# Kernel tuning notes

Measured on AMD Instinct MI355X. Metric: run time of the kernel, lower is better.

Reference implementation:

```python
import jax, jax.numpy as jnp
import numpy as np

N_HEADS = 16
EMBED_DIM = 1024
HEAD_DIM = EMBED_DIM // N_HEADS  # 64
SRC_LEN = 64  # shifted-causal mask: key j visible iff j <= i + SRC_LEN
THETA = 10000.0


def _rope_tables(T, D, dtype):
    # angles[t, p] = t / theta^(2p/D), p in [0, D/2)
    freqs = 1.0 / (THETA ** (jnp.arange(0, D, 2, dtype=jnp.float32) / D))  # [D/2]
    ang = jnp.arange(T, dtype=jnp.float32)[:, None] * freqs[None, :]       # [T, D/2]
    return jnp.cos(ang).astype(dtype), jnp.sin(ang).astype(dtype)


def _apply_rope(x, cos, sin):
    # x: [B, T, H, D]; pairs along last dim act as complex numbers
    B, T, H, D = x.shape
    xp = x.reshape(B, T, H, D // 2, 2)
    x0, x1 = xp[..., 0], xp[..., 1]
    c = cos[None, :, None, :]  # [1, T, 1, D/2]
    s = sin[None, :, None, :]
    o0 = x0 * c - x1 * s
    o1 = x0 * s + x1 * c
    return jnp.stack([o0, o1], axis=-1).reshape(B, T, H, D)


def setup_inputs() -> dict:
    key = jax.random.key(0)
    ks = jax.random.split(key, 9)
    B, T, C = 2, 2048, EMBED_DIM
    sc = 1.0 / np.sqrt(C)
    inp = {
        "x_1": jax.random.normal(ks[0], (B, T, C), dtype=jnp.float32),
        "x_2": jax.random.normal(ks[1], (B, T, C), dtype=jnp.float32),
        "wq": jax.random.normal(ks[2], (C, C), dtype=jnp.float32) * sc,
        "bq": jax.random.normal(ks[3], (C,), dtype=jnp.float32) * sc,
        "wk": jax.random.normal(ks[4], (C, C), dtype=jnp.float32) * sc,
        "bk": jax.random.normal(ks[5], (C,), dtype=jnp.float32) * sc,
        "wv": jax.random.normal(ks[6], (C, C), dtype=jnp.float32) * sc,
        "bv": jax.random.normal(ks[7], (C,), dtype=jnp.float32) * sc,
        "wp": jax.random.normal(ks[8], (C, C), dtype=jnp.float32) * sc,
    }
    return inp


def reference(x_1, x_2, wq, bq, wk, bk, wv, bv, wp):
    B, T, C = x_1.shape
    H, D = N_HEADS, HEAD_DIM
    q = (x_1 @ wq.T + bq).reshape(B, T, H, D)
    k = (x_2 @ wk.T + bk).reshape(B, T, H, D)
    v = (x_2 @ wv.T + bv).reshape(B, T, H, D)
    cos, sin = _rope_tables(T, D, x_1.dtype)
    q = _apply_rope(q, cos, sin)
    k = _apply_rope(k, cos, sin)
    # attention with shifted causal mask
    attn = jnp.einsum("bihd,bjhd->bhij", q, k) * (D ** -0.5)
    i = jnp.arange(T)
    mask = i[None, :] <= i[:, None] + SRC_LEN  # [T, T], True = visible
    attn = jnp.where(mask[None, None, :, :], attn, -jnp.inf)
    attn = jax.nn.softmax(attn, axis=-1)
    out = jnp.einsum("bhij,bjhd->bihd", attn, v).reshape(B, T, C)
    return out @ wp.T
```

## Files before the change

kernel.cpp:

```cpp
#include <hip/hip_runtime.h>
#include <hip/hip_bf16.h>

typedef __bf16 v8bf __attribute__((ext_vector_type(8)));
typedef float  v4f  __attribute__((ext_vector_type(4)));

#define T_LEN 2048
#define NH 16
#define HD 64
#define BH 32
#define C_DIM 1024
#define SCQ 0.1803368801111737f

#define WS_X1B  ((size_t)0)
#define WS_X2B  ((size_t)8  << 20)
#define WS_W    ((size_t)16 << 20)
#define WS_CTAB ((size_t)24 << 20)
#define WS_STAB (WS_CTAB + 262144)
#define WS_Q    ((size_t)25 << 20)
#define WS_K    ((size_t)33 << 20)
#define WS_VT   ((size_t)41 << 20)
#define WS_O    ((size_t)0)

__device__ __forceinline__ unsigned short f2bf(float f) {
  unsigned int u = __float_as_uint(f);
  u += 0x7fffu + ((u >> 16) & 1u);
  return (unsigned short)(u >> 16);
}
__device__ __forceinline__ float bf2f(unsigned short h) {
  return __uint_as_float(((unsigned int)h) << 16);
}

__device__ __forceinline__ float xg_max(float m) {
  m = fmaxf(m, __shfl_xor(m, 16, 64));
  m = fmaxf(m, __shfl_xor(m, 32, 64));
  return m;
}
__device__ __forceinline__ float xg_sum(float m) {
  m = m + __shfl_xor(m, 16, 64);
  m = m + __shfl_xor(m, 32, 64);
  return m;
}
__device__ __forceinline__ unsigned int packbf2(float lo, float hi) {
  return (unsigned int)f2bf(lo) | ((unsigned int)f2bf(hi) << 16);
}

__global__ __launch_bounds__(256) void cvt_kernel(
    const float* __restrict__ x1, const float* __restrict__ x2,
    const float* __restrict__ wq, const float* __restrict__ wk,
    const float* __restrict__ wv, const float* __restrict__ wp,
    unsigned short* __restrict__ x1b, unsigned short* __restrict__ x2b,
    unsigned short* __restrict__ wqb) {
  int i = blockIdx.x * 256 + threadIdx.x;
  if (i >= 3145728) return;
  const float* s; unsigned short* d; int off;
  if (i < 1048576) { s = x1; d = x1b; off = i; }
  else if (i < 2097152) { s = x2; d = x2b; off = i - 1048576; }
  else {
    int j = i - 2097152;
    int w = j >> 18;
    off = j & 262143;
    s = (w == 0) ? wq : (w == 1) ? wk : (w == 2) ? wv : wp;
    d = wqb + ((size_t)w * 1048576);
  }
  float4 v = ((const float4*)s)[off];
  ushort4 o;
  o.x = f2bf(v.x); o.y = f2bf(v.y); o.z = f2bf(v.z); o.w = f2bf(v.w);
  ((ushort4*)d)[off] = o;
}

__global__ __launch_bounds__(256) void tab_kernel(float* __restrict__ ctab,
                                                  float* __restrict__ stab) {
  int i = blockIdx.x * 256 + threadIdx.x;
  int t = i >> 5, f = i & 31;
  float freq = powf(10000.0f, -(float)f * (1.0f / 32.0f));
  float a = (float)t * freq;
  ctab[i] = cosf(a);
  stab[i] = sinf(a);
}

__global__ __launch_bounds__(256) void qk_gemm(
    const unsigned short* __restrict__ x1b, const unsigned short* __restrict__ x2b,
    const unsigned short* __restrict__ wall,
    const float* __restrict__ bq, const float* __restrict__ bk,
    const float* __restrict__ ctab, const float* __restrict__ stab,
    unsigned short* __restrict__ Qd, unsigned short* __restrict__ Kd) {
  int z = blockIdx.z;
  const unsigned short* A = (z == 0) ? x1b : x2b;
  const unsigned short* W = wall + (size_t)z * 1048576;
  const float* bias = (z == 0) ? bq : bk;
  unsigned short* dst = (z == 0) ? Qd : Kd;
  float scale = (z == 0) ? SCQ : 1.0f;

  __shared__ unsigned short lds[2][8192];
  int tid = threadIdx.x;
  int wave = tid >> 6, lane = tid & 63;
  int wm = wave >> 1, wn = wave & 1;
  int r = lane & 15, g = lane >> 4;
  int phys = blockIdx.y * (int)gridDim.x + blockIdx.x;
  int logical = (phys & 7) * 32 + (phys >> 3);
  int m0 = (logical >> 3) * 128, n0 = (logical & 7) * 128;
  int s3 = r & 3;

  v4f zero = {0.f, 0.f, 0.f, 0.f};
  v4f acc[4][4];
#pragma unroll
  for (int i = 0; i < 4; ++i)
#pragma unroll
    for (int j = 0; j < 4; ++j) acc[i][j] = zero;

  auto stage = [&](int b, int k0) {
    const unsigned short* Ab = A + (size_t)m0 * 1024 + k0;
    const unsigned short* Bb = W + (size_t)n0 * 1024 + k0;
#pragma unroll
    for (int it = 0; it < 2; ++it) {
      int c = it * 256 + tid;
      int row = c >> 2;
      int sc = (c & 3) ^ (row & 3);
      __builtin_amdgcn_global_load_lds(
          (const __attribute__((address_space(1))) void*)(Ab + (size_t)row * 1024 + sc * 8),
          (__attribute__((address_space(3))) void*)(&lds[b][0] + it * 2048 + wave * 512),
          16, 0, 0);
      __builtin_amdgcn_global_load_lds(
          (const __attribute__((address_space(1))) void*)(Bb + (size_t)row * 1024 + sc * 8),
          (__attribute__((address_space(3))) void*)(&lds[b][4096] + it * 2048 + wave * 512),
          16, 0, 0);
    }
  };

  stage(0, 0);
  asm volatile("s_waitcnt vmcnt(0)");
  __syncthreads();
  int cur = 0;

  for (int k0 = 0; k0 < 1024; k0 += 32) {
    if (k0 + 32 < 1024) stage(cur ^ 1, k0 + 32);
    v8bf af[4], bfr[4];
#pragma unroll
    for (int mf = 0; mf < 4; ++mf)
      af[mf] = *(const v8bf*)(&lds[cur][0] + (wm * 64 + mf * 16 + r) * 32 + ((g ^ s3) << 3));
#pragma unroll
    for (int nf = 0; nf < 4; ++nf)
      bfr[nf] = *(const v8bf*)(&lds[cur][4096] + (wn * 64 + nf * 16 + r) * 32 + ((g ^ s3) << 3));
#pragma unroll
    for (int mf = 0; mf < 4; ++mf)
#pragma unroll
      for (int nf = 0; nf < 4; ++nf)
        acc[mf][nf] = __builtin_amdgcn_mfma_f32_16x16x32_bf16(bfr[nf], af[mf], acc[mf][nf], 0, 0, 0);
    asm volatile("s_waitcnt vmcnt(0)");
    __syncthreads();
    cur ^= 1;
  }

#pragma unroll
  for (int mf = 0; mf < 4; ++mf) {
    int t = m0 + wm * 64 + mf * 16 + r;
    int b = t >> 11, tt = t & 2047;
#pragma unroll
    for (int nf = 0; nf < 4; ++nf) {
      int c0 = n0 + wn * 64 + nf * 16 + g * 4;
      int h = c0 >> 6, dh = c0 & 63;
      float4 b4 = *(const float4*)(bias + c0);
      int f0 = (dh >> 1);
      float2 cp = *(const float2*)(ctab + tt * 32 + f0);
      float2 sp = *(const float2*)(stab + tt * 32 + f0);
      float x0 = acc[mf][nf][0] + b4.x, x1 = acc[mf][nf][1] + b4.y;
      float x2 = acc[mf][nf][2] + b4.z, x3 = acc[mf][nf][3] + b4.w;
      ushort4 pk;
      pk.x = f2bf((x0 * cp.x - x1 * sp.x) * scale);
      pk.y = f2bf((x0 * sp.x + x1 * cp.x) * scale);
      pk.z = f2bf((x2 * cp.y - x3 * sp.y) * scale);
      pk.w = f2bf((x2 * sp.y + x3 * cp.y) * scale);
      *(ushort4*)(dst + (((size_t)(b * NH + h)) * T_LEN + tt) * HD + dh) = pk;
    }
  }
}

__global__ __launch_bounds__(256) void v_gemm(
    const unsigned short* __restrict__ x2b, const unsigned short* __restrict__ wv,
    const float* __restrict__ bv, unsigned short* __restrict__ VTd) {
  __shared__ unsigned short lds[2][8192];
  int tid = threadIdx.x;
  int wave = tid >> 6, lane = tid & 63;
  int wm = wave >> 1, wn = wave & 1;
  int r = lane & 15, g = lane >> 4;
  int phys = blockIdx.y * (int)gridDim.x + blockIdx.x;
  int logical = (phys & 7) * 32 + (phys >> 3);
  int m0 = (logical >> 3) * 128, n0 = (logical & 7) * 128;
  int s3 = r & 3;

  v4f zero = {0.f, 0.f, 0.f, 0.f};
  v4f acc[4][4];
#pragma unroll
  for (int i = 0; i < 4; ++i)
#pragma unroll
    for (int j = 0; j < 4; ++j) acc[i][j] = zero;

  auto stage = [&](int b, int k0) {
    const unsigned short* Ab = x2b + (size_t)m0 * 1024 + k0;
    const unsigned short* Bb = wv + (size_t)n0 * 1024 + k0;
#pragma unroll
    for (int it = 0; it < 2; ++it) {
      int c = it * 256 + tid;
      int row = c >> 2;
      int sc = (c & 3) ^ (row & 3);
      __builtin_amdgcn_global_load_lds(
          (const __attribute__((address_space(1))) void*)(Ab + (size_t)row * 1024 + sc * 8),
          (__attribute__((address_space(3))) void*)(&lds[b][0] + it * 2048 + wave * 512),
          16, 0, 0);
      __builtin_amdgcn_global_load_lds(
          (const __attribute__((address_space(1))) void*)(Bb + (size_t)row * 1024 + sc * 8),
          (__attribute__((address_space(3))) void*)(&lds[b][4096] + it * 2048 + wave * 512),
          16, 0, 0);
    }
  };

  stage(0, 0);
  asm volatile("s_waitcnt vmcnt(0)");
  __syncthreads();
  int cur = 0;

  for (int k0 = 0; k0 < 1024; k0 += 32) {
    if (k0 + 32 < 1024) stage(cur ^ 1, k0 + 32);
    v8bf af[4], bfr[4];
#pragma unroll
    for (int mf = 0; mf < 4; ++mf)
      af[mf] = *(const v8bf*)(&lds[cur][0] + (wm * 64 + mf * 16 + r) * 32 + ((g ^ s3) << 3));
#pragma unroll
    for (int nf = 0; nf < 4; ++nf)
      bfr[nf] = *(const v8bf*)(&lds[cur][4096] + (wn * 64 + nf * 16 + r) * 32 + ((g ^ s3) << 3));
#pragma unroll
    for (int mf = 0; mf < 4; ++mf)
#pragma unroll
      for (int nf = 0; nf < 4; ++nf)
        acc[mf][nf] = __builtin_amdgcn_mfma_f32_16x16x32_bf16(af[mf], bfr[nf], acc[mf][nf], 0, 0, 0);
    asm volatile("s_waitcnt vmcnt(0)");
    __syncthreads();
    cur ^= 1;
  }
#pragma unroll
  for (int nf = 0; nf < 4; ++nf) {
    int col = n0 + wn * 64 + nf * 16 + r;
    float bv_ = bv[col];
    int h = col >> 6, d = col & 63;
#pragma unroll
    for (int mf = 0; mf < 4; ++mf) {
      int row0 = m0 + wm * 64 + mf * 16 + g * 4;
      int b = row0 >> 11, t0 = row0 & 2047;
      ushort4 pk;
      pk.x = f2bf(acc[mf][nf][0] + bv_);
      pk.y = f2bf(acc[mf][nf][1] + bv_);
      pk.z = f2bf(acc[mf][nf][2] + bv_);
      pk.w = f2bf(acc[mf][nf][3] + bv_);
      *(ushort4*)(VTd + (((size_t)(b * NH + h)) * HD + d) * T_LEN + t0) = pk;
    }
  }
}

__global__ __launch_bounds__(256, 2) void attn_kernel(
    const unsigned short* __restrict__ Qd, const unsigned short* __restrict__ Kd,
    const unsigned short* __restrict__ VTd, unsigned short* __restrict__ Od) {
  int bh = blockIdx.x;
  int qt = (int)gridDim.y - 1 - (int)blockIdx.y;
  int tid = threadIdx.x, wave = tid >> 6, lane = tid & 63;
  int r = lane & 15, g = lane >> 4;
  int qb = qt * 128 + wave * 32;
  const unsigned short* Qp = Qd + (size_t)bh * T_LEN * HD;
  const unsigned short* Kp = Kd + (size_t)bh * T_LEN * HD;
  const unsigned short* Vp = VTd + (size_t)bh * HD * T_LEN;

  __shared__ unsigned short kv[2][2][4096];
  __shared__ unsigned short plds[4][1024];

  v8bf qf[2][2];
#pragma unroll
  for (int qs = 0; qs < 2; ++qs)
#pragma unroll
    for (int c = 0; c < 2; ++c)
      qf[qs][c] = *(const v8bf*)(Qp + (size_t)(qb + qs * 16 + r) * HD + c * 32 + g * 8);

  v4f zero = {0.f, 0.f, 0.f, 0.f};
  v4f oacc[2][4];
#pragma unroll
  for (int qs = 0; qs < 2; ++qs)
#pragma unroll
    for (int dt = 0; dt < 4; ++dt) oacc[qs][dt] = zero;
  float mi[2] = {-1e30f, -1e30f};
  float li[2] = {0.f, 0.f};

  int ktiles = 2 * qt + 3; if (ktiles > 32) ktiles = 32;

  auto stage = [&](int b, int kt) {
    int j0 = kt * 64;
    const unsigned short* Kt = Kp + (size_t)j0 * HD;
#pragma unroll
    for (int is = 0; is < 2; ++is) {
      int q = is * 256 + tid;
      int row = q >> 3, c = q & 7;
      int swc = (c ^ (row & 7)) << 3;
      __builtin_amdgcn_global_load_lds(
          (const __attribute__((address_space(1))) void*)(Kt + row * 64 + swc),
          (__attribute__((address_space(3))) void*)(&kv[b][0][0] + is * 2048 + wave * 512),
          16, 0, 0);
      __builtin_amdgcn_global_load_lds(
          (const __attribute__((address_space(1))) void*)(Vp + (size_t)row * T_LEN + j0 + swc),
          (__attribute__((address_space(3))) void*)(&kv[b][1][0] + is * 2048 + wave * 512),
          16, 0, 0);
    }
  };

  stage(0, 0);
  asm volatile("s_waitcnt vmcnt(0)");
  __syncthreads();
  int cur = 0;

  unsigned short* plw = &plds[wave][0];
  int s7 = r & 7;
  int s8 = s7 << 3;

  for (int kt = 0; kt < ktiles; ++kt) {
    if (kt + 1 < ktiles) stage(cur ^ 1, kt + 1);
    int j0 = kt * 64;
    const unsigned short* kb = &kv[cur][0][0];
    const unsigned short* vb = &kv[cur][1][0];
    v8bf kf0[4], kf1[4], vf0[4], vf1[4];
#pragma unroll
    for (int nt = 0; nt < 4; ++nt) {
      int row = (nt * 16 + r) * 64;
      kf0[nt] = *(const v8bf*)(kb + row + ((g ^ s7) << 3));
      kf1[nt] = *(const v8bf*)(kb + row + (((4 + g) ^ s7) << 3));
      vf0[nt] = *(const v8bf*)(vb + row + ((g ^ s7) << 3));
      vf1[nt] = *(const v8bf*)(vb + row + (((4 + g) ^ s7) << 3));
    }
#pragma unroll
    for (int qs = 0; qs < 2; ++qs) {
      int qmin = qb + qs * 16;
      if (j0 > qmin + 79) continue;
      v4f s[4];
#pragma unroll
      for (int nt = 0; nt < 4; ++nt) {
        v4f a = zero;
        a = __builtin_amdgcn_mfma_f32_16x16x32_bf16(kf0[nt], qf[qs][0], a, 0, 0, 0);
        a = __builtin_amdgcn_mfma_f32_16x16x32_bf16(kf1[nt], qf[qs][1], a, 0, 0, 0);
        s[nt] = a;
      }
      if (j0 + 63 > qmin + 64) {
        int qi64 = qmin + r + 64;
#pragma unroll
        for (int nt = 0; nt < 4; ++nt)
#pragma unroll
          for (int rg = 0; rg < 4; ++rg) {
            int kj = j0 + nt * 16 + g * 4 + rg;
            if (kj > qi64) s[nt][rg] = -1e30f;
          }
      }
      float m = s[0][0];
#pragma unroll
      for (int nt = 0; nt < 4; ++nt)
#pragma unroll
        for (int rg = 0; rg < 4; ++rg) m = fmaxf(m, s[nt][rg]);
      m = xg_max(m);
      float mn = fmaxf(mi[qs], m);
      float al = exp2f(mi[qs] - mn);
      mi[qs] = mn;
      float rs = 0.f;
#pragma unroll
      for (int nt = 0; nt < 4; ++nt)
#pragma unroll
        for (int rg = 0; rg < 4; ++rg) {
          float p = exp2f(s[nt][rg] - mn);
          s[nt][rg] = p;
          rs += p;
        }
      li[qs] = li[qs] * al + rs;
#pragma unroll
      for (int dt = 0; dt < 4; ++dt) oacc[qs][dt] *= al;
#pragma unroll
      for (int nt = 0; nt < 4; ++nt) {
        uint2 w2;
        w2.x = packbf2(s[nt][0], s[nt][1]);
        w2.y = packbf2(s[nt][2], s[nt][3]);
        *(uint2*)(plw + r * 64 + (((nt << 4) + (g << 2)) ^ s8)) = w2;
      }
      v8bf pb0 = *(const v8bf*)(plw + r * 64 + ((g ^ s7) << 3));
      v8bf pb1 = *(const v8bf*)(plw + r * 64 + (((4 + g) ^ s7) << 3));
#pragma unroll
      for (int dt = 0; dt < 4; ++dt) {
        oacc[qs][dt] = __builtin_amdgcn_mfma_f32_16x16x32_bf16(vf0[dt], pb0, oacc[qs][dt], 0, 0, 0);
        oacc[qs][dt] = __builtin_amdgcn_mfma_f32_16x16x32_bf16(vf1[dt], pb1, oacc[qs][dt], 0, 0, 0);
      }
    }
    asm volatile("s_waitcnt vmcnt(0)");
    __syncthreads();
    cur ^= 1;
  }
#pragma unroll
  for (int qs = 0; qs < 2; ++qs) {
    float rli = 1.0f / xg_sum(li[qs]);
#pragma unroll
    for (int dt = 0; dt < 4; ++dt) {
      ushort4 pk;
      pk.x = f2bf(oacc[qs][dt][0] * rli);
      pk.y = f2bf(oacc[qs][dt][1] * rli);
      pk.z = f2bf(oacc[qs][dt][2] * rli);
      pk.w = f2bf(oacc[qs][dt][3] * rli);
      *(ushort4*)(Od + ((size_t)bh * T_LEN + qb + qs * 16 + r) * HD + dt * 16 + g * 4) = pk;
    }
  }
}

__global__ __launch_bounds__(256) void proj_gemm(
    const unsigned short* __restrict__ Ob, const unsigned short* __restrict__ Wpb,
    float* __restrict__ out) {
  __shared__ unsigned short lds[2][8192];
  int tid = threadIdx.x;
  int wave = tid >> 6, lane = tid & 63;
  int wm = wave >> 1, wn = wave & 1;
  int r = lane & 15, g = lane >> 4;
  int phys = blockIdx.y * (int)gridDim.x + blockIdx.x;
  int logical = (phys & 7) * 32 + (phys >> 3);
  int m0 = (logical >> 3) * 128, n0 = (logical & 7) * 128;
  int s3 = r & 3;

  v4f zero = {0.f, 0.f, 0.f, 0.f};
  v4f acc[4][4];
#pragma unroll
  for (int i = 0; i < 4; ++i)
#pragma unroll
    for (int j = 0; j < 4; ++j) acc[i][j] = zero;

  auto stage = [&](int b, int k0) {
    int h = k0 >> 6;
#pragma unroll
    for (int it = 0; it < 2; ++it) {
      int c = it * 256 + tid;
      int row = c >> 2;
      int sc = (c & 3) ^ (row & 3);
      int k = k0 + sc * 8;
      int d = k & 63;
      int mrow = m0 + row;
      int bb = mrow >> 11, t = mrow & 2047;
      __builtin_amdgcn_global_load_lds(
          (const __attribute__((address_space(1))) void*)(Ob + (((size_t)(bb * NH + h)) * T_LEN + t) * HD + d),
          (__attribute__((address_space(3))) void*)(&lds[b][0] + it * 2048 + wave * 512),
          16, 0, 0);
      __builtin_amdgcn_global_load_lds(
          (const __attribute__((address_space(1))) void*)(Wpb + (size_t)(n0 + row) * 1024 + k),
          (__attribute__((address_space(3))) void*)(&lds[b][4096] + it * 2048 + wave * 512),
          16, 0, 0);
    }
  };

  stage(0, 0);
  asm volatile("s_waitcnt vmcnt(0)");
  __syncthreads();
  int cur = 0;

  for (int k0 = 0; k0 < 1024; k0 += 32) {
    if (k0 + 32 < 1024) stage(cur ^ 1, k0 + 32);
    v8bf af[4], bfr[4];
#pragma unroll
    for (int mf = 0; mf < 4; ++mf)
      af[mf] = *(const v8bf*)(&lds[cur][0] + (wm * 64 + mf * 16 + r) * 32 + ((g ^ s3) << 3));
#pragma unroll
    for (int nf = 0; nf < 4; ++nf)
      bfr[nf] = *(const v8bf*)(&lds[cur][4096] + (wn * 64 + nf * 16 + r) * 32 + ((g ^ s3) << 3));
#pragma unroll
    for (int mf = 0; mf < 4; ++mf)
#pragma unroll
      for (int nf = 0; nf < 4; ++nf)
        acc[mf][nf] = __builtin_amdgcn_mfma_f32_16x16x32_bf16(af[mf], bfr[nf], acc[mf][nf], 0, 0, 0);
    asm volatile("s_waitcnt vmcnt(0)");
    __syncthreads();
    cur ^= 1;
  }
#pragma unroll
  for (int mf = 0; mf < 4; ++mf)
#pragma unroll
    for (int nf = 0; nf < 4; ++nf) {
      int col = n0 + wn * 64 + nf * 16 + r;
      int row0 = m0 + wm * 64 + mf * 16 + g * 4;
#pragma unroll
      for (int rg = 0; rg < 4; ++rg)
        out[(size_t)(row0 + rg) * 1024 + col] = acc[mf][nf][rg];
    }
}

extern "C" void kernel_launch(void* const* d_in, const int* in_sizes, int n_in,
                              void* d_out, int out_size, void* d_ws, size_t ws_size,
                              hipStream_t stream) {
  const float* x1 = (const float*)d_in[0];
  const float* x2 = (const float*)d_in[1];
  const float* wq = (const float*)d_in[2];
  const float* bq = (const float*)d_in[3];
  const float* wk = (const float*)d_in[4];
  const float* bk = (const float*)d_in[5];
  const float* wv = (const float*)d_in[6];
  const float* bv = (const float*)d_in[7];
  const float* wp = (const float*)d_in[8];
  float* out = (float*)d_out;
  char* ws = (char*)d_ws;

  unsigned short* x1b = (unsigned short*)(ws + WS_X1B);
  unsigned short* x2b = (unsigned short*)(ws + WS_X2B);
  unsigned short* wqb = (unsigned short*)(ws + WS_W);
  unsigned short* wvb = wqb + 2 * 1048576;
  unsigned short* wpb = wqb + 3 * 1048576;
  float* ctab = (float*)(ws + WS_CTAB);
  float* stab = (float*)(ws + WS_STAB);
  unsigned short* Qd = (unsigned short*)(ws + WS_Q);
  unsigned short* Kd = (unsigned short*)(ws + WS_K);
  unsigned short* VTd = (unsigned short*)(ws + WS_VT);
  unsigned short* Od = (unsigned short*)(ws + WS_O);

  cvt_kernel<<<12288, 256, 0, stream>>>(x1, x2, wq, wk, wv, wp, x1b, x2b, wqb);
  tab_kernel<<<256, 256, 0, stream>>>(ctab, stab);
  qk_gemm<<<dim3(8, 32, 2), 256, 0, stream>>>(x1b, x2b, wqb, bq, bk, ctab, stab, Qd, Kd);
  v_gemm<<<dim3(8, 32), 256, 0, stream>>>(x2b, wvb, bv, VTd);
  attn_kernel<<<dim3(32, 16), 256, 0, stream>>>(Qd, Kd, VTd, Od);
  proj_gemm<<<dim3(8, 32), 256, 0, stream>>>(Od, wpb, out);
}
```

Baseline: 154.2 us.

## Halve attention query tile per block to double grid and use hardware bf16 converts

The attention kernel now gives each wave 16 query rows instead of 32, so a block covers 64 queries and the grid doubles to 32x32 blocks. The per-wave inner loop over two query sub-tiles goes away and register pressure drops. The aim is more parallelism and occupancy for the causal workload on many CUs. In exchange, each K/V tile loaded into LDS serves half as many queries, so K/V global traffic roughly doubles. P and output packing also switch from manual rounding to native __bf16 conversion.

```diff
diff --git a/kernel.cpp b/kernel.cpp
--- a/kernel.cpp
+++ b/kernel.cpp
@@ -40,8 +40,10 @@
   m = m + __shfl_xor(m, 32, 64);
   return m;
 }
-__device__ __forceinline__ unsigned int packbf2(float lo, float hi) {
-  return (unsigned int)f2bf(lo) | ((unsigned int)f2bf(hi) << 16);
+__device__ __forceinline__ unsigned int packbf2hw(float lo, float hi) {
+  unsigned short a = __builtin_bit_cast(unsigned short, (__bf16)lo);
+  unsigned short b = __builtin_bit_cast(unsigned short, (__bf16)hi);
+  return (unsigned int)a | ((unsigned int)b << 16);
 }
 
 __global__ __launch_bounds__(256) void cvt_kernel(
@@ -263,7 +265,7 @@
   int qt = (int)gridDim.y - 1 - (int)blockIdx.y;
   int tid = threadIdx.x, wave = tid >> 6, lane = tid & 63;
   int r = lane & 15, g = lane >> 4;
-  int qb = qt * 128 + wave * 32;
+  int qmin = qt * 64 + wave * 16;
   const unsigned short* Qp = Qd + (size_t)bh * T_LEN * HD;
   const unsigned short* Kp = Kd + (size_t)bh * T_LEN * HD;
   const unsigned short* Vp = VTd + (size_t)bh * HD * T_LEN;
@@ -271,23 +273,17 @@
   __shared__ unsigned short kv[2][2][4096];
   __shared__ unsigned short plds[4][1024];
 
-  v8bf qf[2][2];
-#pragma unroll
-  for (int qs = 0; qs < 2; ++qs)
-#pragma unroll
-    for (int c = 0; c < 2; ++c)
-      qf[qs][c] = *(const v8bf*)(Qp + (size_t)(qb + qs * 16 + r) * HD + c * 32 + g * 8);
+  v8bf qf0 = *(const v8bf*)(Qp + (size_t)(qmin + r) * HD + g * 8);
+  v8bf qf1 = *(const v8bf*)(Qp + (size_t)(qmin + r) * HD + 32 + g * 8);
 
   v4f zero = {0.f, 0.f, 0.f, 0.f};
-  v4f oacc[2][4];
-#pragma unroll
-  for (int qs = 0; qs < 2; ++qs)
-#pragma unroll
-    for (int dt = 0; dt < 4; ++dt) oacc[qs][dt] = zero;
-  float mi[2] = {-1e30f, -1e30f};
-  float li[2] = {0.f, 0.f};
-
-  int ktiles = 2 * qt + 3; if (ktiles > 32) ktiles = 32;
+  v4f oacc[4];
+#pragma unroll
+  for (int dt = 0; dt < 4; ++dt) oacc[dt] = zero;
+  float mi = -1e30f;
+  float li = 0.f;
+
+  int ktiles = qt + 2; if (ktiles > 32) ktiles = 32;
 
   auto stage = [&](int b, int kt) {
     int j0 = kt * 64;
@@ -331,80 +327,72 @@
       vf0[nt] = *(const v8bf*)(vb + row + ((g ^ s7) << 3));
       vf1[nt] = *(const v8bf*)(vb + row + (((4 + g) ^ s7) << 3));
     }
-#pragma unroll
-    for (int qs = 0; qs < 2; ++qs) {
-      int qmin = qb + qs * 16;
-      if (j0 > qmin + 79) continue;
-      v4f s[4];
-#pragma unroll
-      for (int nt = 0; nt < 4; ++nt) {
-        v4f a = zero;
-        a = __builtin_amdgcn_mfma_f32_16x16x32_bf16(kf0[nt], qf[qs][0], a, 0, 0, 0);
-        a = __builtin_amdgcn_mfma_f32_16x16x32_bf16(kf1[nt], qf[qs][1], a, 0, 0, 0);
-        s[nt] = a;
+    v4f s[4];
+#pragma unroll
+    for (int nt = 0; nt < 4; ++nt) {
+      v4f a = zero;
+      a = __builtin_amdgcn_mfma_f32_16x16x32_bf16(kf0[nt], qf0, a, 0, 0, 0);
+      a = __builtin_amdgcn_mfma_f32_16x16x32_bf16(kf1[nt], qf1, a, 0, 0, 0);
+      s[nt] = a;
+    }
+    if (j0 + 63 > qmin + 64) {
+      int qi64 = qmin + r + 64;
+#pragma unroll
+      for (int nt = 0; nt < 4; ++nt)
+#pragma unroll
+        for (int rg = 0; rg < 4; ++rg) {
+          int kj = j0 + nt * 16 + g * 4 + rg;
+          if (kj > qi64) s[nt][rg] = -1e30f;
+        }
+    }
+    float m = s[0][0];
+#pragma unroll
+    for (int nt = 0; nt < 4; ++nt)
+#pragma unroll
+      for (int rg = 0; rg < 4; ++rg) m = fmaxf(m, s[nt][rg]);
+    m = xg_max(m);
+    float mn = fmaxf(mi, m);
+    float al = exp2f(mi - mn);
+    mi = mn;
+    float rs = 0.f;
+#pragma unroll
+    for (int nt = 0; nt < 4; ++nt)
+#pragma unroll
+      for (int rg = 0; rg < 4; ++rg) {
+        float p = exp2f(s[nt][rg] - mn);
+        s[nt][rg] = p;
+        rs += p;
       }
-      if (j0 + 63 > qmin + 64) {
-        int qi64 = qmin + r + 64;
-#pragma unroll
-        for (int nt = 0; nt < 4; ++nt)
-#pragma unroll
-          for (int rg = 0; rg < 4; ++rg) {
-            int kj = j0 + nt * 16 + g * 4 + rg;
-            if (kj > qi64) s[nt][rg] = -1e30f;
-          }
-      }
-      float m = s[0][0];
-#pragma unroll
-      for (int nt = 0; nt < 4; ++nt)
-#pragma unroll
-        for (int rg = 0; rg < 4; ++rg) m = fmaxf(m, s[nt][rg]);
-      m = xg_max(m);
-      float mn = fmaxf(mi[qs], m);
-      float al = exp2f(mi[qs] - mn);
-      mi[qs] = mn;
-      float rs = 0.f;
-#pragma unroll
-      for (int nt = 0; nt < 4; ++nt)
-#pragma unroll
-        for (int rg = 0; rg < 4; ++rg) {
-          float p = exp2f(s[nt][rg] - mn);
-          s[nt][rg] = p;
-          rs += p;
-        }
-      li[qs] = li[qs] * al + rs;
-#pragma unroll
-      for (int dt = 0; dt < 4; ++dt) oacc[qs][dt] *= al;
-#pragma unroll
-      for (int nt = 0; nt < 4; ++nt) {
-        uint2 w2;
-        w2.x = packbf2(s[nt][0], s[nt][1]);
-        w2.y = packbf2(s[nt][2], s[nt][3]);
-        *(uint2*)(plw + r * 64 + (((nt << 4) + (g << 2)) ^ s8)) = w2;
-      }
-      v8bf pb0 = *(const v8bf*)(plw + r * 64 + ((g ^ s7) << 3));
-      v8bf pb1 = *(const v8bf*)(plw + r * 64 + (((4 + g) ^ s7) << 3));
-#pragma unroll
-      for (int dt = 0; dt < 4; ++dt) {
-        oacc[qs][dt] = __builtin_amdgcn_mfma_f32_16x16x32_bf16(vf0[dt], pb0, oacc[qs][dt], 0, 0, 0);
-        oacc[qs][dt] = __builtin_amdgcn_mfma_f32_16x16x32_bf16(vf1[dt], pb1, oacc[qs][dt], 0, 0, 0);
-      }
+    li = li * al + rs;
+#pragma unroll
+    for (int dt = 0; dt < 4; ++dt) oacc[dt] *= al;
+#pragma unroll
+    for (int nt = 0; nt < 4; ++nt) {
+      uint2 w2;
+      w2.x = packbf2hw(s[nt][0], s[nt][1]);
+      w2.y = packbf2hw(s[nt][2], s[nt][3]);
+      *(uint2*)(plw + r * 64 + (((nt << 4) + (g << 2)) ^ s8)) = w2;
+    }
+    v8bf pb0 = *(const v8bf*)(plw + r * 64 + ((g ^ s7) << 3));
+    v8bf pb1 = *(const v8bf*)(plw + r * 64 + (((4 + g) ^ s7) << 3));
+#pragma unroll
+    for (int dt = 0; dt < 4; ++dt) {
+      oacc[dt] = __builtin_amdgcn_mfma_f32_16x16x32_bf16(vf0[dt], pb0, oacc[dt], 0, 0, 0);
+      oacc[dt] = __builtin_amdgcn_mfma_f32_16x16x32_bf16(vf1[dt], pb1, oacc[dt], 0, 0, 0);
     }
     asm volatile("s_waitcnt vmcnt(0)");
     __syncthreads();
     cur ^= 1;
   }
-#pragma unroll
-  for (int qs = 0; qs < 2; ++qs) {
-    float rli = 1.0f / xg_sum(li[qs]);
-#pragma unroll
-    for (int dt = 0; dt < 4; ++dt) {
-      ushort4 pk;
-      pk.x = f2bf(oacc[qs][dt][0] * rli);
-      pk.y = f2bf(oacc[qs][dt][1] * rli);
-      pk.z = f2bf(oacc[qs][dt][2] * rli);
-      pk.w = f2bf(oacc[qs][dt][3] * rli);
-      *(ushort4*)(Od + ((size_t)bh * T_LEN + qb + qs * 16 + r) * HD + dt * 16 + g * 4) = pk;
-    }
+  float rli = 1.0f / xg_sum(li);
+#pragma unroll
+  for (int dt = 0; dt < 4; ++dt) {
+    ushort4 pk;
+    pk.x = __builtin_bit_cast(unsigned short, (__bf16)(oacc[dt][0] * rli));
+    pk.y = __builtin_bit_cast(unsigned short, (__bf16)(oacc[dt][1] * rli));
+    pk.z = __builtin_bit_cast(unsigned short, (__bf16)(oacc[dt][2] * rli));
+    pk.w = __builtin_bit_cast(unsigned short, (__bf16)(oacc[dt][3] * rli));
+    *(ushort4*)(Od + ((size_t)bh * T_LEN + qmin + r) * HD + dt * 16 + g * 4) = pk;
   }
 }
 
@@ -516,6 +504,6 @@
   tab_kernel<<<256, 256, 0, stream>>>(ctab, stab);
   qk_gemm<<<dim3(8, 32, 2), 256, 0, stream>>>(x1b, x2b, wqb, bq, bk, ctab, stab, Qd, Kd);
   v_gemm<<<dim3(8, 32), 256, 0, stream>>>(x2b, wvb, bv, VTd);
-  attn_kernel<<<dim3(32, 16), 256, 0, stream>>>(Qd, Kd, VTd, Od);
+  attn_kernel<<<dim3(32, 32), 256, 0, stream>>>(Qd, Kd, VTd, Od);
   proj_gemm<<<dim3(8, 32), 256, 0, stream>>>(Od, wpb, out);
 }
```

After: 134.4 us. 12.8% less time.
